# Performance work log

Measured on AMD Instinct MI355X. Metric: run time of the kernel, lower is better.

Reference implementation:

```python
import jax, jax.numpy as jnp
import numpy as np

E = 8          # num_experts
H = 2048       # hidden_size
D = 4096       # expert_dim
R = 8          # lora rank
SCALE = 16.0 / 8.0  # lora_alpha / r
T = 2048       # tokens per expert


def setup_inputs() -> dict:
    key = jax.random.key(0)
    ks = jax.random.split(key, 7)
    s = lambda *shape: 1.0 / np.sqrt(shape[-1])
    hidden_states = jax.random.normal(ks[0], (E * T, H), dtype=jnp.float32)
    # base weights (nn.Linear convention: [out, in]) stacked over experts
    W_gu = jax.random.normal(ks[1], (E, 2 * D, H), dtype=jnp.float32) * s(H)
    W_d = jax.random.normal(ks[2], (E, H, D), dtype=jnp.float32) * s(D)
    # LoRA factors: A [r, in] (kaiming-ish), B [out, r] (zeros in training init;
    # use small random here so the delta path is exercised)
    A_gu = jax.random.normal(ks[3], (E, R, H), dtype=jnp.float32) * s(H)
    B_gu = jax.random.normal(ks[4], (E, 2 * D, R), dtype=jnp.float32) * 0.01
    A_d = jax.random.normal(ks[5], (E, R, D), dtype=jnp.float32) * s(D)
    B_d = jax.random.normal(ks[6], (E, H, R), dtype=jnp.float32) * 0.01
    return {"hidden_states": hidden_states, "W_gu": W_gu, "A_gu": A_gu,
            "B_gu": B_gu, "W_d": W_d, "A_d": A_d, "B_d": B_d}


def _lora_linear(x, W, A, B):
    # x: [e, t, in]; W: [e, out, in]; A: [e, r, in]; B: [e, out, r]
    base = jnp.einsum('eti,eoi->eto', x, W)
    low = jnp.einsum('eti,eri->etr', x, A)        # skinny projection
    delta = jnp.einsum('etr,eor->eto', low, B)
    return base + SCALE * delta


def reference(hidden_states, W_gu, A_gu, B_gu, W_d, A_d, B_d):
    x = hidden_states.reshape(E, -1, H)           # [E, T, H]
    gate_up = _lora_linear(x, W_gu, A_gu, B_gu)   # [E, T, 2D]
    gate, up = gate_up[..., :D], gate_up[..., D:]
    h = up * jax.nn.silu(gate)                    # SwiGLU [E, T, D]
    out = _lora_linear(h, W_d, A_d, B_d)          # [E, T, H]
    return out.reshape(-1, H)
```

## Files before the change

### kernel.cpp

```cpp
#include <hip/hip_runtime.h>
#include <hip/hip_bf16.h>

#define E_ 8
#define H_ 2048
#define D_ 4096
#define R_ 8
#define T_ 2048
#define TWO_D_ 8192
#define SCALE_ 2.0f

typedef __attribute__((ext_vector_type(8))) short short8;
typedef __attribute__((ext_vector_type(4))) float f32x4;

__device__ __forceinline__ unsigned short f2bf(float f) {
  union { float f; unsigned u; } c; c.f = f;
  unsigned u = c.u + 0x7fffu + ((c.u >> 16) & 1u);
  return (unsigned short)(u >> 16);
}
__device__ __forceinline__ float bf2f(unsigned short s) {
  union { unsigned u; float f; } c; c.u = ((unsigned)s) << 16;
  return c.f;
}

__device__ __forceinline__ void gl16(const void* g, void* l) {
  __builtin_amdgcn_global_load_lds(
      (const __attribute__((address_space(1))) void*)g,
      (__attribute__((address_space(3))) void*)l, 16, 0, 0);
}

__device__ __forceinline__ int lds_off(int rr, int ks, int lq) {
  return (((rr >> 5) & 3) << 13) | (((rr >> 7) & 1) << 12) | ((rr & 31) << 7) | (ks << 6) | (lq << 4);
}

template <int K, bool XBF16, bool WRITEXB>
__global__ __launch_bounds__(256) void k_low(const void* __restrict__ Xv,
                                             const float* __restrict__ A,
                                             float* __restrict__ low,
                                             unsigned short* __restrict__ xbout) {
  int wave = (blockIdx.x * 256 + threadIdx.x) >> 6;
  int lane = threadIdx.x & 63;
  int e = wave >> 11;
  const float* Ae = A + (long)e * R_ * K;
  float acc[R_] = {0.f,0.f,0.f,0.f,0.f,0.f,0.f,0.f};
  for (int it = 0; it < K / 256; ++it) {
    int i = it * 256 + lane * 4;
    float xv[4];
    if constexpr (!XBF16) {
      const float* x = (const float*)Xv + (long)wave * K;
      f32x4 v = *(const f32x4*)(x + i);
      xv[0]=v[0]; xv[1]=v[1]; xv[2]=v[2]; xv[3]=v[3];
      if constexpr (WRITEXB) {
        ushort4 u; u.x=f2bf(xv[0]); u.y=f2bf(xv[1]); u.z=f2bf(xv[2]); u.w=f2bf(xv[3]);
        *(ushort4*)(xbout + (long)wave * K + i) = u;
      }
    } else {
      const unsigned short* x = (const unsigned short*)Xv + (long)wave * K;
      ushort4 u = *(const ushort4*)(x + i);
      xv[0]=bf2f(u.x); xv[1]=bf2f(u.y); xv[2]=bf2f(u.z); xv[3]=bf2f(u.w);
    }
    #pragma unroll
    for (int r = 0; r < R_; ++r) {
      f32x4 a = *(const f32x4*)(Ae + r * K + i);
      acc[r] += xv[0]*a[0] + xv[1]*a[1] + xv[2]*a[2] + xv[3]*a[3];
    }
  }
  #pragma unroll
  for (int r = 0; r < R_; ++r) {
    float v = acc[r];
    #pragma unroll
    for (int off = 32; off > 0; off >>= 1) v += __shfl_xor(v, off);
    acc[r] = v;
  }
  if (lane == 0) {
    #pragma unroll
    for (int r = 0; r < R_; ++r) low[(long)wave * R_ + r] = acc[r];
  }
}

__global__ __launch_bounds__(256) void k_f2bf(const float* __restrict__ src,
                                              unsigned short* __restrict__ dst,
                                              long n) {
  long i = ((long)blockIdx.x * 256 + threadIdx.x) * 8;
  long stride = (long)gridDim.x * 256 * 8;
  for (; i < n; i += stride) {
    f32x4 a = *(const f32x4*)(src + i);
    f32x4 b = *(const f32x4*)(src + i + 4);
    ushort4 lo, hi;
    lo.x=f2bf(a[0]); lo.y=f2bf(a[1]); lo.z=f2bf(a[2]); lo.w=f2bf(a[3]);
    hi.x=f2bf(b[0]); hi.y=f2bf(b[1]); hi.z=f2bf(b[2]); hi.w=f2bf(b[3]);
    *(ushort4*)(dst + i) = lo;
    *(ushort4*)(dst + i + 4) = hi;
  }
}

__global__ __launch_bounds__(512, 2) void k_gemm1_8p(
    const unsigned short* __restrict__ Xb, const unsigned short* __restrict__ Wb,
    const float* __restrict__ Bgu, const float* __restrict__ low,
    unsigned short* __restrict__ Hout) {
  __shared__ __align__(16) char lds[131072];

  const int MT = T_ / 256, NT = D_ / 128;
  int b = blockIdx.x;
  int cpx = (int)gridDim.x >> 3;
  int swz = (b & 7) * cpx + (b >> 3);
  int e  = swz / (MT * NT);
  int r0 = swz % (MT * NT);
  int nt = r0 / MT, mt = r0 % MT;

  int tid = threadIdx.x, lane = tid & 63;
  int wid = tid >> 6, wm = wid >> 2, wn = wid & 3;
  int lrow = lane & 15, lq = lane >> 4;
  int X4 = (lrow & 7) << 4;
  const int NKT = H_ / 64;

  unsigned ro = (unsigned)tid * 16;
  unsigned so = ro ^ (((ro >> 7) & 7u) << 4);
  int sh = (so >> 12) & 1, sr = (so >> 7) & 31, sc = (so & 127) >> 1;
  const unsigned short* pA[4]; const unsigned short* pB[4];
  #pragma unroll
  for (int q = 0; q < 4; ++q) {
    long arow = (long)e * T_ + mt * 256 + sh * 128 + q * 32 + sr;
    pA[q] = Xb + arow * H_ + sc;
    long wrow = sh ? ((long)e * TWO_D_ + D_ + nt * 128 + q * 32 + sr)
                   : ((long)e * TWO_D_ +      nt * 128 + q * 32 + sr);
    pB[q] = Wb + wrow * (long)H_ + sc;
  }
  auto SA = [&](int d, int q) { gl16(pA[q], lds + d * 32768 + q * 8192 + ro); pA[q] += 64; };
  auto SB = [&](int d, int q) { gl16(pB[q], lds + 65536 + d * 32768 + q * 8192 + ro); pB[q] += 64; };

  f32x4 accg[2][8] = {}, accu[2][8] = {};
  short8 BG[2][2], BU[2][2], af[2][2];

  SA(0,0); SB(0,0); SA(0,1); SB(0,1); SA(0,2); SB(0,2); SA(0,3); SB(0,3);
  SA(1,0); SB(1,0); SA(1,1); SB(1,1); SA(1,2); SB(1,2);
  asm volatile("s_waitcnt vmcnt(6)" ::: "memory");
  __builtin_amdgcn_s_barrier();

  int rbA = wm * 128 + lrow;
  for (int t = 0; t < NKT; ++t) {
    int d = t & 1;
    const char* Ab = lds + d * 32768;
    const char* Bb = lds + 65536 + d * 32768;

#define G1_MFMA(q)                                                                   \
    __builtin_amdgcn_s_setprio(1);                                                   \
    _Pragma("unroll") for (int m2 = 0; m2 < 2; ++m2)                                 \
      _Pragma("unroll") for (int ks = 0; ks < 2; ++ks)                               \
        _Pragma("unroll") for (int nj = 0; nj < 2; ++nj) {                           \
          accg[nj][(q)*2+m2] = __builtin_amdgcn_mfma_f32_16x16x32_bf16(              \
              BG[nj][ks], af[m2][ks], accg[nj][(q)*2+m2], 0, 0, 0);                  \
          accu[nj][(q)*2+m2] = __builtin_amdgcn_mfma_f32_16x16x32_bf16(              \
              BU[nj][ks], af[m2][ks], accu[nj][(q)*2+m2], 0, 0, 0);                  \
        }                                                                            \
    __builtin_amdgcn_s_setprio(0);

#define G1_LDA(q)                                                                    \
    _Pragma("unroll") for (int m2 = 0; m2 < 2; ++m2)                                 \
      _Pragma("unroll") for (int ks = 0; ks < 2; ++ks)                               \
        af[m2][ks] = *(const short8*)(Ab + (lds_off(rbA + ((q)*2+m2)*16, ks, lq) ^ X4));

#define G1_SYNC()                                                                    \
    __builtin_amdgcn_s_barrier();                                                    \
    asm volatile("s_waitcnt lgkmcnt(0)" ::: "memory");                               \
    __builtin_amdgcn_sched_barrier(0);

    #pragma unroll
    for (int nj = 0; nj < 2; ++nj)
      #pragma unroll
      for (int ks = 0; ks < 2; ++ks) {
        int rg = wn * 32 + nj * 16 + lrow;
        BG[nj][ks] = *(const short8*)(Bb + (lds_off(rg, ks, lq) ^ X4));
        BU[nj][ks] = *(const short8*)(Bb + (lds_off(rg + 128, ks, lq) ^ X4));
      }
    G1_LDA(0);
    if (t + 1 < NKT) { SA(d ^ 1, 3); SB(d ^ 1, 3); }
    G1_SYNC();
    G1_MFMA(0);
    __builtin_amdgcn_s_barrier();
    G1_LDA(1);
    if (t + 2 < NKT) { SA(d, 0); SB(d, 0); }
    G1_SYNC();
    G1_MFMA(1);
    __builtin_amdgcn_s_barrier();
    G1_LDA(2);
    if (t + 2 < NKT) { SA(d, 1); SB(d, 1); }
    G1_SYNC();
    G1_MFMA(2);
    __builtin_amdgcn_s_barrier();
    G1_LDA(3);
    if (t + 2 < NKT) {
      SA(d, 2); SB(d, 2);
      asm volatile("s_waitcnt vmcnt(6)" ::: "memory");
    } else {
      asm volatile("s_waitcnt vmcnt(0)" ::: "memory");
    }
    G1_SYNC();
    G1_MFMA(3);
    __builtin_amdgcn_s_barrier();
  }

  __syncthreads();
  unsigned short* sLo2 = (unsigned short*)lds;
  unsigned short* sB2  = (unsigned short*)(lds + 16384);
  {
    short8 z = {};
    if (tid < 256) {
      const float* lp = low + ((long)e * T_ + mt * 256 + tid) * R_;
      short8 v;
      #pragma unroll
      for (int r = 0; r < 8; ++r) ((unsigned short*)&v)[r] = f2bf(SCALE_ * lp[r]);
      *(short8*)(sLo2 + tid * 32) = v;
      *(short8*)(sLo2 + tid * 32 + 8) = z;
      *(short8*)(sLo2 + tid * 32 + 16) = z;
      *(short8*)(sLo2 + tid * 32 + 24) = z;
    } else {
      int r = tid - 256;
      long wrow = (r < 128) ? ((long)e * TWO_D_ + nt * 128 + r)
                            : ((long)e * TWO_D_ + D_ + nt * 128 + (r - 128));
      const float* bp = Bgu + wrow * R_;
      short8 v;
      #pragma unroll
      for (int k = 0; k < 8; ++k) ((unsigned short*)&v)[k] = f2bf(bp[k]);
      *(short8*)(sB2 + r * 32) = v;
      *(short8*)(sB2 + r * 32 + 8) = z;
      *(short8*)(sB2 + r * 32 + 16) = z;
      *(short8*)(sB2 + r * 32 + 24) = z;
    }
  }
  __syncthreads();
  {
    #pragma unroll
    for (int mi = 0; mi < 8; ++mi) {
      short8 alo = *(const short8*)(sLo2 + (rbA + mi * 16) * 32 + lq * 8);
      #pragma unroll
      for (int nj = 0; nj < 2; ++nj) {
        int rg = wn * 32 + nj * 16 + lrow;
        short8 bg2 = *(const short8*)(sB2 + rg * 32 + lq * 8);
        short8 bu2 = *(const short8*)(sB2 + (rg + 128) * 32 + lq * 8);
        accg[nj][mi] = __builtin_amdgcn_mfma_f32_16x16x32_bf16(bg2, alo, accg[nj][mi], 0, 0, 0);
        accu[nj][mi] = __builtin_amdgcn_mfma_f32_16x16x32_bf16(bu2, alo, accu[nj][mi], 0, 0, 0);
      }
    }
  }
  unsigned short* sT = (unsigned short*)(lds + 32768);
  #pragma unroll
  for (int mi = 0; mi < 8; ++mi) {
    int tl = rbA + mi * 16;
    #pragma unroll
    for (int nj = 0; nj < 2; ++nj) {
      int cb = wn * 32 + nj * 16 + lq * 4;
      ushort4 o;
      #pragma unroll
      for (int j = 0; j < 4; ++j) {
        float gate = accg[nj][mi][j];
        float up   = accu[nj][mi][j];
        float hh = up * (gate / (1.f + __expf(-gate)));
        (&o.x)[j] = f2bf(hh);
      }
      *(ushort4*)(sT + tl * 136 + cb) = o;
    }
  }
  __syncthreads();
  {
    long base = ((long)e * T_ + mt * 256) * D_ + nt * 128;
    int rr2 = tid >> 4, cc2 = (tid & 15) * 8;
    #pragma unroll
    for (int p = 0; p < 8; ++p) {
      int r = p * 32 + rr2;
      short8 v = *(const short8*)(sT + r * 136 + cc2);
      *(short8*)(Hout + base + (long)r * D_ + cc2) = v;
    }
  }
}

__global__ __launch_bounds__(512, 2) void k_gemm2_8p(
    const unsigned short* __restrict__ Hin, const unsigned short* __restrict__ Wdb,
    const float* __restrict__ Bd, const float* __restrict__ low,
    float* __restrict__ Out) {
  __shared__ __align__(16) char lds[131072];

  const int MT = T_ / 256, NT = H_ / 256;
  int b = blockIdx.x;
  int cpx = (int)gridDim.x >> 3;
  int swz = (b & 7) * cpx + (b >> 3);
  int e  = swz / (MT * NT);
  int r0 = swz % (MT * NT);
  int nt = r0 / MT, mt = r0 % MT;

  int tid = threadIdx.x, lane = tid & 63;
  int wid = tid >> 6, wm = wid >> 2, wn = wid & 3;
  int lrow = lane & 15, lq = lane >> 4;
  int X4 = (lrow & 7) << 4;
  const int NKT = D_ / 64;

  unsigned ro = (unsigned)tid * 16;
  unsigned so = ro ^ (((ro >> 7) & 7u) << 4);
  int sh = (so >> 12) & 1, sr = (so >> 7) & 31, sc = (so & 127) >> 1;
  const unsigned short* pA[4]; const unsigned short* pB[4];
  #pragma unroll
  for (int q = 0; q < 4; ++q) {
    long arow = (long)e * T_ + mt * 256 + sh * 128 + q * 32 + sr;
    pA[q] = Hin + arow * D_ + sc;
    long wrow = (long)e * H_ + nt * 256 + sh * 128 + q * 32 + sr;
    pB[q] = Wdb + wrow * (long)D_ + sc;
  }
  auto SA = [&](int d, int q) { gl16(pA[q], lds + d * 32768 + q * 8192 + ro); pA[q] += 64; };
  auto SB = [&](int d, int q) { gl16(pB[q], lds + 65536 + d * 32768 + q * 8192 + ro); pB[q] += 64; };

  f32x4 acc[8][4] = {};
  short8 BF[4][2], af[2][2];

  SA(0,0); SB(0,0); SA(0,1); SB(0,1); SA(0,2); SB(0,2); SA(0,3); SB(0,3);
  SA(1,0); SB(1,0); SA(1,1); SB(1,1); SA(1,2); SB(1,2);
  asm volatile("s_waitcnt vmcnt(6)" ::: "memory");
  __builtin_amdgcn_s_barrier();

  int rbA = wm * 128 + lrow;
  for (int t = 0; t < NKT; ++t) {
    int d = t & 1;
    const char* Ab = lds + d * 32768;
    const char* Bb = lds + 65536 + d * 32768;

#define G2_MFMA(q)                                                                   \
    __builtin_amdgcn_s_setprio(1);                                                   \
    _Pragma("unroll") for (int m2 = 0; m2 < 2; ++m2)                                 \
      _Pragma("unroll") for (int ks = 0; ks < 2; ++ks)                               \
        _Pragma("unroll") for (int ni = 0; ni < 4; ++ni)                             \
          acc[(q)*2+m2][ni] = __builtin_amdgcn_mfma_f32_16x16x32_bf16(               \
              af[m2][ks], BF[ni][ks], acc[(q)*2+m2][ni], 0, 0, 0);                   \
    __builtin_amdgcn_s_setprio(0);

#define G2_LDA(q)                                                                    \
    _Pragma("unroll") for (int m2 = 0; m2 < 2; ++m2)                                 \
      _Pragma("unroll") for (int ks = 0; ks < 2; ++ks)                               \
        af[m2][ks] = *(const short8*)(Ab + (lds_off(rbA + ((q)*2+m2)*16, ks, lq) ^ X4));

    #pragma unroll
    for (int ni = 0; ni < 4; ++ni)
      #pragma unroll
      for (int ks = 0; ks < 2; ++ks)
        BF[ni][ks] = *(const short8*)(Bb + (lds_off(wn * 64 + ni * 16 + lrow, ks, lq) ^ X4));
    G2_LDA(0);
    if (t + 1 < NKT) { SA(d ^ 1, 3); SB(d ^ 1, 3); }
    __builtin_amdgcn_s_barrier();
    asm volatile("s_waitcnt lgkmcnt(0)" ::: "memory");
    __builtin_amdgcn_sched_barrier(0);
    G2_MFMA(0);
    __builtin_amdgcn_s_barrier();
    G2_LDA(1);
    if (t + 2 < NKT) { SA(d, 0); SB(d, 0); }
    __builtin_amdgcn_s_barrier();
    asm volatile("s_waitcnt lgkmcnt(0)" ::: "memory");
    __builtin_amdgcn_sched_barrier(0);
    G2_MFMA(1);
    __builtin_amdgcn_s_barrier();
    G2_LDA(2);
    if (t + 2 < NKT) { SA(d, 1); SB(d, 1); }
    __builtin_amdgcn_s_barrier();
    asm volatile("s_waitcnt lgkmcnt(0)" ::: "memory");
    __builtin_amdgcn_sched_barrier(0);
    G2_MFMA(2);
    __builtin_amdgcn_s_barrier();
    G2_LDA(3);
    if (t + 2 < NKT) {
      SA(d, 2); SB(d, 2);
      asm volatile("s_waitcnt vmcnt(6)" ::: "memory");
    } else {
      asm volatile("s_waitcnt vmcnt(0)" ::: "memory");
    }
    __builtin_amdgcn_s_barrier();
    asm volatile("s_waitcnt lgkmcnt(0)" ::: "memory");
    __builtin_amdgcn_sched_barrier(0);
    G2_MFMA(3);
    __builtin_amdgcn_s_barrier();
  }

  __syncthreads();
  unsigned short* sLo2 = (unsigned short*)lds;
  unsigned short* sB2  = (unsigned short*)(lds + 16384);
  {
    short8 z = {};
    if (tid < 256) {
      const float* lp = low + ((long)e * T_ + mt * 256 + tid) * R_;
      short8 v;
      #pragma unroll
      for (int r = 0; r < 8; ++r) ((unsigned short*)&v)[r] = f2bf(SCALE_ * lp[r]);
      *(short8*)(sLo2 + tid * 32) = v;
      *(short8*)(sLo2 + tid * 32 + 8) = z;
      *(short8*)(sLo2 + tid * 32 + 16) = z;
      *(short8*)(sLo2 + tid * 32 + 24) = z;
    } else {
      int r = tid - 256;
      const float* bp = Bd + ((long)e * H_ + nt * 256 + r) * R_;
      short8 v;
      #pragma unroll
      for (int k = 0; k < 8; ++k) ((unsigned short*)&v)[k] = f2bf(bp[k]);
      *(short8*)(sB2 + r * 32) = v;
      *(short8*)(sB2 + r * 32 + 8) = z;
      *(short8*)(sB2 + r * 32 + 16) = z;
      *(short8*)(sB2 + r * 32 + 24) = z;
    }
  }
  __syncthreads();
  #pragma unroll
  for (int mi = 0; mi < 8; ++mi) {
    short8 alo = *(const short8*)(sLo2 + (rbA + mi * 16) * 32 + lq * 8);
    #pragma unroll
    for (int ni = 0; ni < 4; ++ni) {
      short8 bd2 = *(const short8*)(sB2 + (wn * 64 + ni * 16 + lrow) * 32 + lq * 8);
      acc[mi][ni] = __builtin_amdgcn_mfma_f32_16x16x32_bf16(alo, bd2, acc[mi][ni], 0, 0, 0);
    }
  }
  {
    long rowbase = (long)e * T_ + mt * 256 + wm * 128;
    int colbase = nt * 256 + wn * 64;
    #pragma unroll
    for (int mi = 0; mi < 8; ++mi)
      #pragma unroll
      for (int j = 0; j < 4; ++j) {
        long row = rowbase + mi * 16 + lq * 4 + j;
        #pragma unroll
        for (int ni = 0; ni < 4; ++ni)
          Out[row * H_ + colbase + ni * 16 + lrow] = acc[mi][ni][j];
      }
  }
}

extern "C" void kernel_launch(void* const* d_in, const int* in_sizes, int n_in,
                              void* d_out, int out_size, void* d_ws, size_t ws_size,
                              hipStream_t stream) {
  const float* x   = (const float*)d_in[0];
  const float* Wgu = (const float*)d_in[1];
  const float* Agu = (const float*)d_in[2];
  const float* Bgu = (const float*)d_in[3];
  const float* Wd  = (const float*)d_in[4];
  const float* Ad  = (const float*)d_in[5];
  const float* Bd  = (const float*)d_in[6];
  float* out = (float*)d_out;

  char* ws = (char*)d_ws;
  const size_t SZ_H   = (size_t)E_ * T_ * D_ * 2;
  const size_t SZ_LOW = (size_t)E_ * T_ * R_ * 4;
  const size_t SZ_XB  = (size_t)E_ * T_ * H_ * 2;
  const size_t SZ_WGU = (size_t)E_ * TWO_D_ * H_ * 2;

  unsigned short* hbuf = (unsigned short*)ws;
  float* low1 = (float*)(ws + SZ_H);
  float* low2 = (float*)(ws + SZ_H + SZ_LOW);
  unsigned short* xb   = (unsigned short*)(ws + SZ_H + 2 * SZ_LOW);
  unsigned short* wgub = (unsigned short*)(ws + SZ_H + 2 * SZ_LOW + SZ_XB);
  unsigned short* wdb  = (unsigned short*)(ws + SZ_H + 2 * SZ_LOW + SZ_XB + SZ_WGU);

  hipLaunchKernelGGL((k_low<H_, false, true>), dim3(E_ * T_ / 4), dim3(256), 0, stream,
                     (const void*)x, Agu, low1, xb);
  hipLaunchKernelGGL(k_f2bf, dim3(2048), dim3(256), 0, stream, Wgu, wgub, (long)E_ * TWO_D_ * H_);
  hipLaunchKernelGGL(k_f2bf, dim3(2048), dim3(256), 0, stream, Wd,  wdb,  (long)E_ * H_ * D_);
  hipLaunchKernelGGL(k_gemm1_8p, dim3(E_ * (T_ / 256) * (D_ / 128)), dim3(512), 0, stream,
                     xb, wgub, Bgu, low1, hbuf);
  hipLaunchKernelGGL((k_low<D_, true, false>), dim3(E_ * T_ / 4), dim3(256), 0, stream,
                     (const void*)hbuf, Ad, low2, (unsigned short*)nullptr);
  hipLaunchKernelGGL(k_gemm2_8p, dim3(E_ * (T_ / 256) * (H_ / 256)), dim3(512), 0, stream,
                     hbuf, wdb, Bd, low2, out);
}
```

Before: 1.129 ms.

## Fuse fp32-to-bf16 weight conversion into GEMM B-tile loads via registers

Drops the two standalone weight conversion kernels. Each GEMM now loads fp32 weight tiles into registers, converts them with packed bf16 convert instructions, and writes them to LDS inside a restructured software pipeline with adjusted vmcnt waits. This removes a full fp32 read plus bf16 write-and-reread of both weight tensors. In exchange, each GEMM block reads twice as many weight bytes, and weights are re-read and re-converted by every M-tile block (8 per expert), and register pressure rises.

```diff
diff --git a/kernel.cpp b/kernel.cpp
--- a/kernel.cpp
+++ b/kernel.cpp
@@ -77,24 +77,16 @@
   }
 }
 
-__global__ __launch_bounds__(256) void k_f2bf(const float* __restrict__ src,
-                                              unsigned short* __restrict__ dst,
-                                              long n) {
-  long i = ((long)blockIdx.x * 256 + threadIdx.x) * 8;
-  long stride = (long)gridDim.x * 256 * 8;
-  for (; i < n; i += stride) {
-    f32x4 a = *(const f32x4*)(src + i);
-    f32x4 b = *(const f32x4*)(src + i + 4);
-    ushort4 lo, hi;
-    lo.x=f2bf(a[0]); lo.y=f2bf(a[1]); lo.z=f2bf(a[2]); lo.w=f2bf(a[3]);
-    hi.x=f2bf(b[0]); hi.y=f2bf(b[1]); hi.z=f2bf(b[2]); hi.w=f2bf(b[3]);
-    *(ushort4*)(dst + i) = lo;
-    *(ushort4*)(dst + i + 4) = hi;
-  }
-}
+#define CVT_WR(S0, S1, DST)                                                         \
+  { uint4 wv;                                                                       \
+    asm("v_cvt_pk_bf16_f32 %0, %1, %2" : "=v"(wv.x) : "v"((S0)[0]), "v"((S0)[1]));  \
+    asm("v_cvt_pk_bf16_f32 %0, %1, %2" : "=v"(wv.y) : "v"((S0)[2]), "v"((S0)[3]));  \
+    asm("v_cvt_pk_bf16_f32 %0, %1, %2" : "=v"(wv.z) : "v"((S1)[0]), "v"((S1)[1]));  \
+    asm("v_cvt_pk_bf16_f32 %0, %1, %2" : "=v"(wv.w) : "v"((S1)[2]), "v"((S1)[3]));  \
+    *(uint4*)(DST) = wv; }
 
 __global__ __launch_bounds__(512, 2) void k_gemm1_8p(
-    const unsigned short* __restrict__ Xb, const unsigned short* __restrict__ Wb,
+    const unsigned short* __restrict__ Xb, const float* __restrict__ Wgu,
     const float* __restrict__ Bgu, const float* __restrict__ low,
     unsigned short* __restrict__ Hout) {
   __shared__ __align__(16) char lds[131072];
@@ -116,24 +108,43 @@
   unsigned ro = (unsigned)tid * 16;
   unsigned so = ro ^ (((ro >> 7) & 7u) << 4);
   int sh = (so >> 12) & 1, sr = (so >> 7) & 31, sc = (so & 127) >> 1;
-  const unsigned short* pA[4]; const unsigned short* pB[4];
+  const unsigned short* pA[4]; const float* pB[4];
   #pragma unroll
   for (int q = 0; q < 4; ++q) {
     long arow = (long)e * T_ + mt * 256 + sh * 128 + q * 32 + sr;
     pA[q] = Xb + arow * H_ + sc;
     long wrow = sh ? ((long)e * TWO_D_ + D_ + nt * 128 + q * 32 + sr)
                    : ((long)e * TWO_D_ +      nt * 128 + q * 32 + sr);
-    pB[q] = Wb + wrow * (long)H_ + sc;
+    pB[q] = Wgu + wrow * (long)H_ + sc;
   }
   auto SA = [&](int d, int q) { gl16(pA[q], lds + d * 32768 + q * 8192 + ro); pA[q] += 64; };
-  auto SB = [&](int d, int q) { gl16(pB[q], lds + 65536 + d * 32768 + q * 8192 + ro); pB[q] += 64; };
+
+  f32x4 bl[4][2];
+#define G1_IB(s, q) { bl[s][0] = *(const f32x4*)(pB[q]); bl[s][1] = *(const f32x4*)(pB[q] + 4); pB[q] += 64; }
+#define G1_WRB(s, dd, qq) CVT_WR(bl[s][0], bl[s][1], lds + 65536 + (dd) * 32768 + (qq) * 8192 + ro)
 
   f32x4 accg[2][8] = {}, accu[2][8] = {};
   short8 BG[2][2], BU[2][2], af[2][2];
 
-  SA(0,0); SB(0,0); SA(0,1); SB(0,1); SA(0,2); SB(0,2); SA(0,3); SB(0,3);
-  SA(1,0); SB(1,0); SA(1,1); SB(1,1); SA(1,2); SB(1,2);
-  asm volatile("s_waitcnt vmcnt(6)" ::: "memory");
+  {
+    f32x4 pr[7][2];
+    #pragma unroll
+    for (int q = 0; q < 4; ++q) {
+      pr[q][0] = *(const f32x4*)(pB[q]); pr[q][1] = *(const f32x4*)(pB[q] + 4); pB[q] += 64;
+      SA(0, q);
+    }
+    #pragma unroll
+    for (int q = 0; q < 3; ++q) {
+      pr[4 + q][0] = *(const f32x4*)(pB[q]); pr[4 + q][1] = *(const f32x4*)(pB[q] + 4); pB[q] += 64;
+      SA(1, q);
+    }
+    #pragma unroll
+    for (int i = 0; i < 7; ++i) {
+      int dd = (i < 4) ? 0 : 1, qq = (i < 4) ? i : i - 4;
+      CVT_WR(pr[i][0], pr[i][1], lds + 65536 + dd * 32768 + qq * 8192 + ro);
+    }
+  }
+  asm volatile("s_waitcnt vmcnt(0)" ::: "memory");
   __builtin_amdgcn_s_barrier();
 
   int rbA = wm * 128 + lrow;
@@ -164,6 +175,8 @@
     asm volatile("s_waitcnt lgkmcnt(0)" ::: "memory");                               \
     __builtin_amdgcn_sched_barrier(0);
 
+    if (t > 0 && t + 1 < NKT) { G1_WRB(1, d ^ 1, 0); }
+    if (t + 1 < NKT) { G1_IB(0, 3); SA(d ^ 1, 3); }
     #pragma unroll
     for (int nj = 0; nj < 2; ++nj)
       #pragma unroll
@@ -173,27 +186,29 @@
         BU[nj][ks] = *(const short8*)(Bb + (lds_off(rg + 128, ks, lq) ^ X4));
       }
     G1_LDA(0);
-    if (t + 1 < NKT) { SA(d ^ 1, 3); SB(d ^ 1, 3); }
     G1_SYNC();
     G1_MFMA(0);
     __builtin_amdgcn_s_barrier();
+    if (t > 0 && t + 1 < NKT) { G1_WRB(2, d ^ 1, 1); }
+    if (t + 2 < NKT) { G1_IB(1, 0); SA(d, 0); }
     G1_LDA(1);
-    if (t + 2 < NKT) { SA(d, 0); SB(d, 0); }
     G1_SYNC();
     G1_MFMA(1);
     __builtin_amdgcn_s_barrier();
+    if (t > 0 && t + 1 < NKT) { G1_WRB(3, d ^ 1, 2); }
+    if (t + 2 < NKT) { G1_IB(2, 1); SA(d, 1); }
     G1_LDA(2);
-    if (t + 2 < NKT) { SA(d, 1); SB(d, 1); }
     G1_SYNC();
     G1_MFMA(2);
     __builtin_amdgcn_s_barrier();
-    G1_LDA(3);
+    if (t + 1 < NKT) { G1_WRB(0, d ^ 1, 3); }
     if (t + 2 < NKT) {
-      SA(d, 2); SB(d, 2);
-      asm volatile("s_waitcnt vmcnt(6)" ::: "memory");
+      G1_IB(3, 2); SA(d, 2);
+      asm volatile("s_waitcnt vmcnt(9)" ::: "memory");
     } else {
       asm volatile("s_waitcnt vmcnt(0)" ::: "memory");
     }
+    G1_LDA(3);
     G1_SYNC();
     G1_MFMA(3);
     __builtin_amdgcn_s_barrier();
@@ -274,7 +289,7 @@
 }
 
 __global__ __launch_bounds__(512, 2) void k_gemm2_8p(
-    const unsigned short* __restrict__ Hin, const unsigned short* __restrict__ Wdb,
+    const unsigned short* __restrict__ Hin, const float* __restrict__ Wd,
     const float* __restrict__ Bd, const float* __restrict__ low,
     float* __restrict__ Out) {
   __shared__ __align__(16) char lds[131072];
@@ -296,23 +311,42 @@
   unsigned ro = (unsigned)tid * 16;
   unsigned so = ro ^ (((ro >> 7) & 7u) << 4);
   int sh = (so >> 12) & 1, sr = (so >> 7) & 31, sc = (so & 127) >> 1;
-  const unsigned short* pA[4]; const unsigned short* pB[4];
+  const unsigned short* pA[4]; const float* pB[4];
   #pragma unroll
   for (int q = 0; q < 4; ++q) {
     long arow = (long)e * T_ + mt * 256 + sh * 128 + q * 32 + sr;
     pA[q] = Hin + arow * D_ + sc;
     long wrow = (long)e * H_ + nt * 256 + sh * 128 + q * 32 + sr;
-    pB[q] = Wdb + wrow * (long)D_ + sc;
+    pB[q] = Wd + wrow * (long)D_ + sc;
   }
   auto SA = [&](int d, int q) { gl16(pA[q], lds + d * 32768 + q * 8192 + ro); pA[q] += 64; };
-  auto SB = [&](int d, int q) { gl16(pB[q], lds + 65536 + d * 32768 + q * 8192 + ro); pB[q] += 64; };
+
+  f32x4 bl[4][2];
+#define G2_IB(s, q) { bl[s][0] = *(const f32x4*)(pB[q]); bl[s][1] = *(const f32x4*)(pB[q] + 4); pB[q] += 64; }
+#define G2_WRB(s, dd, qq) CVT_WR(bl[s][0], bl[s][1], lds + 65536 + (dd) * 32768 + (qq) * 8192 + ro)
 
   f32x4 acc[8][4] = {};
   short8 BF[4][2], af[2][2];
 
-  SA(0,0); SB(0,0); SA(0,1); SB(0,1); SA(0,2); SB(0,2); SA(0,3); SB(0,3);
-  SA(1,0); SB(1,0); SA(1,1); SB(1,1); SA(1,2); SB(1,2);
-  asm volatile("s_waitcnt vmcnt(6)" ::: "memory");
+  {
+    f32x4 pr[7][2];
+    #pragma unroll
+    for (int q = 0; q < 4; ++q) {
+      pr[q][0] = *(const f32x4*)(pB[q]); pr[q][1] = *(const f32x4*)(pB[q] + 4); pB[q] += 64;
+      SA(0, q);
+    }
+    #pragma unroll
+    for (int q = 0; q < 3; ++q) {
+      pr[4 + q][0] = *(const f32x4*)(pB[q]); pr[4 + q][1] = *(const f32x4*)(pB[q] + 4); pB[q] += 64;
+      SA(1, q);
+    }
+    #pragma unroll
+    for (int i = 0; i < 7; ++i) {
+      int dd = (i < 4) ? 0 : 1, qq = (i < 4) ? i : i - 4;
+      CVT_WR(pr[i][0], pr[i][1], lds + 65536 + dd * 32768 + qq * 8192 + ro);
+    }
+  }
+  asm volatile("s_waitcnt vmcnt(0)" ::: "memory");
   __builtin_amdgcn_s_barrier();
 
   int rbA = wm * 128 + lrow;
@@ -335,42 +369,43 @@
       _Pragma("unroll") for (int ks = 0; ks < 2; ++ks)                               \
         af[m2][ks] = *(const short8*)(Ab + (lds_off(rbA + ((q)*2+m2)*16, ks, lq) ^ X4));
 
+#define G2_SYNC()                                                                    \
+    __builtin_amdgcn_s_barrier();                                                    \
+    asm volatile("s_waitcnt lgkmcnt(0)" ::: "memory");                               \
+    __builtin_amdgcn_sched_barrier(0);
+
+    if (t > 0 && t + 1 < NKT) { G2_WRB(1, d ^ 1, 0); }
+    if (t + 1 < NKT) { G2_IB(0, 3); SA(d ^ 1, 3); }
     #pragma unroll
     for (int ni = 0; ni < 4; ++ni)
       #pragma unroll
       for (int ks = 0; ks < 2; ++ks)
         BF[ni][ks] = *(const short8*)(Bb + (lds_off(wn * 64 + ni * 16 + lrow, ks, lq) ^ X4));
     G2_LDA(0);
-    if (t + 1 < NKT) { SA(d ^ 1, 3); SB(d ^ 1, 3); }
-    __builtin_amdgcn_s_barrier();
-    asm volatile("s_waitcnt lgkmcnt(0)" ::: "memory");
-    __builtin_amdgcn_sched_barrier(0);
+    G2_SYNC();
     G2_MFMA(0);
     __builtin_amdgcn_s_barrier();
+    if (t > 0 && t + 1 < NKT) { G2_WRB(2, d ^ 1, 1); }
+    if (t + 2 < NKT) { G2_IB(1, 0); SA(d, 0); }
     G2_LDA(1);
-    if (t + 2 < NKT) { SA(d, 0); SB(d, 0); }
-    __builtin_amdgcn_s_barrier();
-    asm volatile("s_waitcnt lgkmcnt(0)" ::: "memory");
-    __builtin_amdgcn_sched_barrier(0);
+    G2_SYNC();
     G2_MFMA(1);
     __builtin_amdgcn_s_barrier();
+    if (t > 0 && t + 1 < NKT) { G2_WRB(3, d ^ 1, 2); }
+    if (t + 2 < NKT) { G2_IB(2, 1); SA(d, 1); }
     G2_LDA(2);
-    if (t + 2 < NKT) { SA(d, 1); SB(d, 1); }
-    __builtin_amdgcn_s_barrier();
-    asm volatile("s_waitcnt lgkmcnt(0)" ::: "memory");
-    __builtin_amdgcn_sched_barrier(0);
+    G2_SYNC();
     G2_MFMA(2);
     __builtin_amdgcn_s_barrier();
-    G2_LDA(3);
+    if (t + 1 < NKT) { G2_WRB(0, d ^ 1, 3); }
     if (t + 2 < NKT) {
-      SA(d, 2); SB(d, 2);
-      asm volatile("s_waitcnt vmcnt(6)" ::: "memory");
+      G2_IB(3, 2); SA(d, 2);
+      asm volatile("s_waitcnt vmcnt(9)" ::: "memory");
     } else {
       asm volatile("s_waitcnt vmcnt(0)" ::: "memory");
     }
-    __builtin_amdgcn_s_barrier();
-    asm volatile("s_waitcnt lgkmcnt(0)" ::: "memory");
-    __builtin_amdgcn_sched_barrier(0);
+    G2_LDA(3);
+    G2_SYNC();
     G2_MFMA(3);
     __builtin_amdgcn_s_barrier();
   }
@@ -441,24 +476,18 @@
   char* ws = (char*)d_ws;
   const size_t SZ_H   = (size_t)E_ * T_ * D_ * 2;
   const size_t SZ_LOW = (size_t)E_ * T_ * R_ * 4;
-  const size_t SZ_XB  = (size_t)E_ * T_ * H_ * 2;
-  const size_t SZ_WGU = (size_t)E_ * TWO_D_ * H_ * 2;
 
   unsigned short* hbuf = (unsigned short*)ws;
   float* low1 = (float*)(ws + SZ_H);
   float* low2 = (float*)(ws + SZ_H + SZ_LOW);
   unsigned short* xb   = (unsigned short*)(ws + SZ_H + 2 * SZ_LOW);
-  unsigned short* wgub = (unsigned short*)(ws + SZ_H + 2 * SZ_LOW + SZ_XB);
-  unsigned short* wdb  = (unsigned short*)(ws + SZ_H + 2 * SZ_LOW + SZ_XB + SZ_WGU);
 
   hipLaunchKernelGGL((k_low<H_, false, true>), dim3(E_ * T_ / 4), dim3(256), 0, stream,
                      (const void*)x, Agu, low1, xb);
-  hipLaunchKernelGGL(k_f2bf, dim3(2048), dim3(256), 0, stream, Wgu, wgub, (long)E_ * TWO_D_ * H_);
-  hipLaunchKernelGGL(k_f2bf, dim3(2048), dim3(256), 0, stream, Wd,  wdb,  (long)E_ * H_ * D_);
   hipLaunchKernelGGL(k_gemm1_8p, dim3(E_ * (T_ / 256) * (D_ / 128)), dim3(512), 0, stream,
-                     xb, wgub, Bgu, low1, hbuf);
+                     xb, Wgu, Bgu, low1, hbuf);
   hipLaunchKernelGGL((k_low<D_, true, false>), dim3(E_ * T_ / 4), dim3(256), 0, stream,
                      (const void*)hbuf, Ad, low2, (unsigned short*)nullptr);
   hipLaunchKernelGGL(k_gemm2_8p, dim3(E_ * (T_ / 256) * (H_ / 256)), dim3(512), 0, stream,
-                     hbuf, wdb, Bd, low2, out);
-}
+                     hbuf, Wd, Bd, low2, out);
+}
```

After: 1.280 ms. +13.3%, slower.

## Overlap W_d bf16 conversion with gemm1 and merge preprocessing launches

Applied to the files above, without the earlier changes.

The standalone f32-to-bf16 conversion of W_d is removed. Each gemm1 thread now converts a slice of W_d inside its K-loop, loading one f32x4 and storing it as bf16 over sixteen iterations. The goal is to hide that memory-bound work under the MFMA-bound GEMM. The gate/up LoRA projection, the x conversion and the W_gu conversion are also fused into one launch that splits its blocks by role. The cost is extra VGPRs and memory traffic inside gemm1, which could reduce occupancy or disturb its load pipeline.

```diff
diff --git a/kernel.cpp b/kernel.cpp
--- a/kernel.cpp
+++ b/kernel.cpp
@@ -32,35 +32,73 @@
   return (((rr >> 5) & 3) << 13) | (((rr >> 7) & 1) << 12) | ((rr & 31) << 7) | (ks << 6) | (lq << 4);
 }
 
-template <int K, bool XBF16, bool WRITEXB>
-__global__ __launch_bounds__(256) void k_low(const void* __restrict__ Xv,
-                                             const float* __restrict__ A,
+__global__ __launch_bounds__(256) void k_pre(const float* __restrict__ x,
+                                             const float* __restrict__ Agu,
                                              float* __restrict__ low,
-                                             unsigned short* __restrict__ xbout) {
+                                             unsigned short* __restrict__ xb,
+                                             const float* __restrict__ Wgu,
+                                             unsigned short* __restrict__ wgub) {
+  const int NB_LOW = E_ * T_ / 4;
+  if (blockIdx.x < NB_LOW) {
+    int wave = (blockIdx.x * 256 + threadIdx.x) >> 6;
+    int lane = threadIdx.x & 63;
+    int e = wave >> 11;
+    const float* Ae = Agu + (long)e * R_ * H_;
+    float acc[R_] = {0.f,0.f,0.f,0.f,0.f,0.f,0.f,0.f};
+    for (int it = 0; it < H_ / 256; ++it) {
+      int i = it * 256 + lane * 4;
+      const float* xp = x + (long)wave * H_;
+      f32x4 v = *(const f32x4*)(xp + i);
+      ushort4 u; u.x=f2bf(v[0]); u.y=f2bf(v[1]); u.z=f2bf(v[2]); u.w=f2bf(v[3]);
+      *(ushort4*)(xb + (long)wave * H_ + i) = u;
+      #pragma unroll
+      for (int r = 0; r < R_; ++r) {
+        f32x4 a = *(const f32x4*)(Ae + r * H_ + i);
+        acc[r] += v[0]*a[0] + v[1]*a[1] + v[2]*a[2] + v[3]*a[3];
+      }
+    }
+    #pragma unroll
+    for (int r = 0; r < R_; ++r) {
+      float v = acc[r];
+      #pragma unroll
+      for (int off = 32; off > 0; off >>= 1) v += __shfl_xor(v, off);
+      acc[r] = v;
+    }
+    if (lane == 0) {
+      #pragma unroll
+      for (int r = 0; r < R_; ++r) low[(long)wave * R_ + r] = acc[r];
+    }
+  } else {
+    const long n = (long)E_ * TWO_D_ * H_;
+    long i = ((long)(blockIdx.x - NB_LOW) * 256 + threadIdx.x) * 8;
+    const long stride = (long)1024 * 256 * 8;
+    for (; i < n; i += stride) {
+      f32x4 a = *(const f32x4*)(Wgu + i);
+      f32x4 b = *(const f32x4*)(Wgu + i + 4);
+      ushort4 lo, hi;
+      lo.x=f2bf(a[0]); lo.y=f2bf(a[1]); lo.z=f2bf(a[2]); lo.w=f2bf(a[3]);
+      hi.x=f2bf(b[0]); hi.y=f2bf(b[1]); hi.z=f2bf(b[2]); hi.w=f2bf(b[3]);
+      *(ushort4*)(wgub + i) = lo;
+      *(ushort4*)(wgub + i + 4) = hi;
+    }
+  }
+}
+
+__global__ __launch_bounds__(256) void k_low2(const unsigned short* __restrict__ Hb,
+                                              const float* __restrict__ Ad,
+                                              float* __restrict__ low) {
   int wave = (blockIdx.x * 256 + threadIdx.x) >> 6;
   int lane = threadIdx.x & 63;
   int e = wave >> 11;
-  const float* Ae = A + (long)e * R_ * K;
+  const float* Ae = Ad + (long)e * R_ * D_;
   float acc[R_] = {0.f,0.f,0.f,0.f,0.f,0.f,0.f,0.f};
-  for (int it = 0; it < K / 256; ++it) {
+  for (int it = 0; it < D_ / 256; ++it) {
     int i = it * 256 + lane * 4;
-    float xv[4];
-    if constexpr (!XBF16) {
-      const float* x = (const float*)Xv + (long)wave * K;
-      f32x4 v = *(const f32x4*)(x + i);
-      xv[0]=v[0]; xv[1]=v[1]; xv[2]=v[2]; xv[3]=v[3];
-      if constexpr (WRITEXB) {
-        ushort4 u; u.x=f2bf(xv[0]); u.y=f2bf(xv[1]); u.z=f2bf(xv[2]); u.w=f2bf(xv[3]);
-        *(ushort4*)(xbout + (long)wave * K + i) = u;
-      }
-    } else {
-      const unsigned short* x = (const unsigned short*)Xv + (long)wave * K;
-      ushort4 u = *(const ushort4*)(x + i);
-      xv[0]=bf2f(u.x); xv[1]=bf2f(u.y); xv[2]=bf2f(u.z); xv[3]=bf2f(u.w);
-    }
+    ushort4 u = *(const ushort4*)(Hb + (long)wave * D_ + i);
+    float xv[4] = {bf2f(u.x), bf2f(u.y), bf2f(u.z), bf2f(u.w)};
     #pragma unroll
     for (int r = 0; r < R_; ++r) {
-      f32x4 a = *(const f32x4*)(Ae + r * K + i);
+      f32x4 a = *(const f32x4*)(Ae + r * D_ + i);
       acc[r] += xv[0]*a[0] + xv[1]*a[1] + xv[2]*a[2] + xv[3]*a[3];
     }
   }
@@ -77,26 +115,11 @@
   }
 }
 
-__global__ __launch_bounds__(256) void k_f2bf(const float* __restrict__ src,
-                                              unsigned short* __restrict__ dst,
-                                              long n) {
-  long i = ((long)blockIdx.x * 256 + threadIdx.x) * 8;
-  long stride = (long)gridDim.x * 256 * 8;
-  for (; i < n; i += stride) {
-    f32x4 a = *(const f32x4*)(src + i);
-    f32x4 b = *(const f32x4*)(src + i + 4);
-    ushort4 lo, hi;
-    lo.x=f2bf(a[0]); lo.y=f2bf(a[1]); lo.z=f2bf(a[2]); lo.w=f2bf(a[3]);
-    hi.x=f2bf(b[0]); hi.y=f2bf(b[1]); hi.z=f2bf(b[2]); hi.w=f2bf(b[3]);
-    *(ushort4*)(dst + i) = lo;
-    *(ushort4*)(dst + i + 4) = hi;
-  }
-}
-
 __global__ __launch_bounds__(512, 2) void k_gemm1_8p(
     const unsigned short* __restrict__ Xb, const unsigned short* __restrict__ Wb,
     const float* __restrict__ Bgu, const float* __restrict__ low,
-    unsigned short* __restrict__ Hout) {
+    unsigned short* __restrict__ Hout,
+    const float* __restrict__ WdSrc, unsigned short* __restrict__ WdDst) {
   __shared__ __align__(16) char lds[131072];
 
   const int MT = T_ / 256, NT = D_ / 128;
@@ -112,6 +135,7 @@
   int lrow = lane & 15, lq = lane >> 4;
   int X4 = (lrow & 7) << 4;
   const int NKT = H_ / 64;
+  const long cid = (long)blockIdx.x * 512 + tid;
 
   unsigned ro = (unsigned)tid * 16;
   unsigned so = ro ^ (((ro >> 7) & 7u) << 4);
@@ -130,6 +154,7 @@
 
   f32x4 accg[2][8] = {}, accu[2][8] = {};
   short8 BG[2][2], BU[2][2], af[2][2];
+  f32x4 cr;
 
   SA(0,0); SB(0,0); SA(0,1); SB(0,1); SA(0,2); SB(0,2); SA(0,3); SB(0,3);
   SA(1,0); SB(1,0); SA(1,1); SB(1,1); SA(1,2); SB(1,2);
@@ -194,6 +219,13 @@
     } else {
       asm volatile("s_waitcnt vmcnt(0)" ::: "memory");
     }
+    if (t >= 2 && t <= 17) {
+      ushort4 o; o.x = f2bf(cr[0]); o.y = f2bf(cr[1]); o.z = f2bf(cr[2]); o.w = f2bf(cr[3]);
+      *(ushort4*)(WdDst + ((long)(t - 2) * 1048576 + cid) * 4) = o;
+    }
+    if (t >= 1 && t <= 16) {
+      cr = *(const f32x4*)(WdSrc + ((long)(t - 1) * 1048576 + cid) * 4);
+    }
     G1_SYNC();
     G1_MFMA(3);
     __builtin_amdgcn_s_barrier();
@@ -451,14 +483,11 @@
   unsigned short* wgub = (unsigned short*)(ws + SZ_H + 2 * SZ_LOW + SZ_XB);
   unsigned short* wdb  = (unsigned short*)(ws + SZ_H + 2 * SZ_LOW + SZ_XB + SZ_WGU);
 
-  hipLaunchKernelGGL((k_low<H_, false, true>), dim3(E_ * T_ / 4), dim3(256), 0, stream,
-                     (const void*)x, Agu, low1, xb);
-  hipLaunchKernelGGL(k_f2bf, dim3(2048), dim3(256), 0, stream, Wgu, wgub, (long)E_ * TWO_D_ * H_);
-  hipLaunchKernelGGL(k_f2bf, dim3(2048), dim3(256), 0, stream, Wd,  wdb,  (long)E_ * H_ * D_);
+  hipLaunchKernelGGL(k_pre, dim3(E_ * T_ / 4 + 1024), dim3(256), 0, stream,
+                     x, Agu, low1, xb, Wgu, wgub);
   hipLaunchKernelGGL(k_gemm1_8p, dim3(E_ * (T_ / 256) * (D_ / 128)), dim3(512), 0, stream,
-                     xb, wgub, Bgu, low1, hbuf);
-  hipLaunchKernelGGL((k_low<D_, true, false>), dim3(E_ * T_ / 4), dim3(256), 0, stream,
-                     (const void*)hbuf, Ad, low2, (unsigned short*)nullptr);
+                     xb, wgub, Bgu, low1, hbuf, Wd, wdb);
+  hipLaunchKernelGGL(k_low2, dim3(E_ * T_ / 4), dim3(256), 0, stream, hbuf, Ad, low2);
   hipLaunchKernelGGL(k_gemm2_8p, dim3(E_ * (T_ / 256) * (H_ / 256)), dim3(512), 0, stream,
                      hbuf, wdb, Bd, low2, out);
 }
```

Result: slower. 1.171 ms (+3.7%).

## Fold LoRA factors into bf16 weights during conversion, drop low-rank passes

Applied to the files above, without the earlier changes.

Computes W + scale·B·A while converting the expert weights to bf16 in one fused preprocessing kernel, also absorbing the activation conversion. This removes both skinny low-rank projection kernels (including the full reread of the intermediate activation) and the rank-8 MFMA epilogues in both GEMMs, and cuts launch count. The LoRA delta is now rounded into the bf16 weight, slightly changing numerics.

```diff
diff --git a/kernel.cpp b/kernel.cpp
--- a/kernel.cpp
+++ b/kernel.cpp
@@ -17,10 +17,6 @@
   unsigned u = c.u + 0x7fffu + ((c.u >> 16) & 1u);
   return (unsigned short)(u >> 16);
 }
-__device__ __forceinline__ float bf2f(unsigned short s) {
-  union { unsigned u; float f; } c; c.u = ((unsigned)s) << 16;
-  return c.f;
-}
 
 __device__ __forceinline__ void gl16(const void* g, void* l) {
   __builtin_amdgcn_global_load_lds(
@@ -32,70 +28,101 @@
   return (((rr >> 5) & 3) << 13) | (((rr >> 7) & 1) << 12) | ((rr & 31) << 7) | (ks << 6) | (lq << 4);
 }
 
-template <int K, bool XBF16, bool WRITEXB>
-__global__ __launch_bounds__(256) void k_low(const void* __restrict__ Xv,
-                                             const float* __restrict__ A,
-                                             float* __restrict__ low,
-                                             unsigned short* __restrict__ xbout) {
-  int wave = (blockIdx.x * 256 + threadIdx.x) >> 6;
-  int lane = threadIdx.x & 63;
-  int e = wave >> 11;
-  const float* Ae = A + (long)e * R_ * K;
-  float acc[R_] = {0.f,0.f,0.f,0.f,0.f,0.f,0.f,0.f};
-  for (int it = 0; it < K / 256; ++it) {
-    int i = it * 256 + lane * 4;
-    float xv[4];
-    if constexpr (!XBF16) {
-      const float* x = (const float*)Xv + (long)wave * K;
-      f32x4 v = *(const f32x4*)(x + i);
-      xv[0]=v[0]; xv[1]=v[1]; xv[2]=v[2]; xv[3]=v[3];
-      if constexpr (WRITEXB) {
-        ushort4 u; u.x=f2bf(xv[0]); u.y=f2bf(xv[1]); u.z=f2bf(xv[2]); u.w=f2bf(xv[3]);
-        *(ushort4*)(xbout + (long)wave * K + i) = u;
+__global__ __launch_bounds__(256) void k_pre(const float* __restrict__ x,
+                                             unsigned short* __restrict__ xb,
+                                             const float* __restrict__ Wgu,
+                                             const float* __restrict__ Agu,
+                                             const float* __restrict__ Bgu,
+                                             unsigned short* __restrict__ wgub,
+                                             const float* __restrict__ Wd,
+                                             const float* __restrict__ Ad,
+                                             const float* __restrict__ Bd,
+                                             unsigned short* __restrict__ wdb) {
+  const int NB_X = 1024, NB_GU = 8192;
+  int bb = blockIdx.x, tid = threadIdx.x;
+  if (bb < NB_X) {
+    const long n = (long)E_ * T_ * H_;
+    long i = ((long)bb * 256 + tid) * 8;
+    const long stride = (long)NB_X * 256 * 8;
+    for (; i < n; i += stride) {
+      f32x4 a = *(const f32x4*)(x + i);
+      f32x4 b = *(const f32x4*)(x + i + 4);
+      ushort4 lo, hi;
+      lo.x=f2bf(a[0]); lo.y=f2bf(a[1]); lo.z=f2bf(a[2]); lo.w=f2bf(a[3]);
+      hi.x=f2bf(b[0]); hi.y=f2bf(b[1]); hi.z=f2bf(b[2]); hi.w=f2bf(b[3]);
+      *(ushort4*)(xb + i) = lo;
+      *(ushort4*)(xb + i + 4) = hi;
+    }
+  } else if (bb < NB_X + NB_GU) {
+    int b2 = bb - NB_X;
+    int e = b2 >> 10;
+    int o8 = (b2 & 1023) * 8;
+    int c = tid * 8;
+    f32x4 a0[8], a1[8];
+    #pragma unroll
+    for (int r = 0; r < 8; ++r) {
+      const float* ap = Agu + ((long)e * R_ + r) * H_ + c;
+      a0[r] = *(const f32x4*)ap;
+      a1[r] = *(const f32x4*)(ap + 4);
+    }
+    #pragma unroll
+    for (int o = 0; o < 8; ++o) {
+      long row = (long)e * TWO_D_ + o8 + o;
+      const float* bp = Bgu + row * R_;
+      const float* wp = Wgu + row * (long)H_ + c;
+      f32x4 w0 = *(const f32x4*)wp;
+      f32x4 w1 = *(const f32x4*)(wp + 4);
+      #pragma unroll
+      for (int r = 0; r < 8; ++r) {
+        float s = SCALE_ * bp[r];
+        w0 += s * a0[r];
+        w1 += s * a1[r];
       }
-    } else {
-      const unsigned short* x = (const unsigned short*)Xv + (long)wave * K;
-      ushort4 u = *(const ushort4*)(x + i);
-      xv[0]=bf2f(u.x); xv[1]=bf2f(u.y); xv[2]=bf2f(u.z); xv[3]=bf2f(u.w);
-    }
-    #pragma unroll
-    for (int r = 0; r < R_; ++r) {
-      f32x4 a = *(const f32x4*)(Ae + r * K + i);
-      acc[r] += xv[0]*a[0] + xv[1]*a[1] + xv[2]*a[2] + xv[3]*a[3];
-    }
-  }
-  #pragma unroll
-  for (int r = 0; r < R_; ++r) {
-    float v = acc[r];
-    #pragma unroll
-    for (int off = 32; off > 0; off >>= 1) v += __shfl_xor(v, off);
-    acc[r] = v;
-  }
-  if (lane == 0) {
-    #pragma unroll
-    for (int r = 0; r < R_; ++r) low[(long)wave * R_ + r] = acc[r];
-  }
-}
-
-__global__ __launch_bounds__(256) void k_f2bf(const float* __restrict__ src,
-                                              unsigned short* __restrict__ dst,
-                                              long n) {
-  long i = ((long)blockIdx.x * 256 + threadIdx.x) * 8;
-  long stride = (long)gridDim.x * 256 * 8;
-  for (; i < n; i += stride) {
-    f32x4 a = *(const f32x4*)(src + i);
-    f32x4 b = *(const f32x4*)(src + i + 4);
-    ushort4 lo, hi;
-    lo.x=f2bf(a[0]); lo.y=f2bf(a[1]); lo.z=f2bf(a[2]); lo.w=f2bf(a[3]);
-    hi.x=f2bf(b[0]); hi.y=f2bf(b[1]); hi.z=f2bf(b[2]); hi.w=f2bf(b[3]);
-    *(ushort4*)(dst + i) = lo;
-    *(ushort4*)(dst + i + 4) = hi;
+      ushort4 lo, hi;
+      lo.x=f2bf(w0[0]); lo.y=f2bf(w0[1]); lo.z=f2bf(w0[2]); lo.w=f2bf(w0[3]);
+      hi.x=f2bf(w1[0]); hi.y=f2bf(w1[1]); hi.z=f2bf(w1[2]); hi.w=f2bf(w1[3]);
+      unsigned short* op = wgub + row * (long)H_ + c;
+      *(ushort4*)op = lo;
+      *(ushort4*)(op + 4) = hi;
+    }
+  } else {
+    int b2 = bb - NB_X - NB_GU;
+    int e = b2 >> 9;
+    int rem = b2 & 511;
+    int h8 = (rem >> 1) * 8;
+    int c = (rem & 1) * 2048 + tid * 8;
+    f32x4 a0[8], a1[8];
+    #pragma unroll
+    for (int r = 0; r < 8; ++r) {
+      const float* ap = Ad + ((long)e * R_ + r) * D_ + c;
+      a0[r] = *(const f32x4*)ap;
+      a1[r] = *(const f32x4*)(ap + 4);
+    }
+    #pragma unroll
+    for (int o = 0; o < 8; ++o) {
+      long row = (long)e * H_ + h8 + o;
+      const float* bp = Bd + row * R_;
+      const float* wp = Wd + row * (long)D_ + c;
+      f32x4 w0 = *(const f32x4*)wp;
+      f32x4 w1 = *(const f32x4*)(wp + 4);
+      #pragma unroll
+      for (int r = 0; r < 8; ++r) {
+        float s = SCALE_ * bp[r];
+        w0 += s * a0[r];
+        w1 += s * a1[r];
+      }
+      ushort4 lo, hi;
+      lo.x=f2bf(w0[0]); lo.y=f2bf(w0[1]); lo.z=f2bf(w0[2]); lo.w=f2bf(w0[3]);
+      hi.x=f2bf(w1[0]); hi.y=f2bf(w1[1]); hi.z=f2bf(w1[2]); hi.w=f2bf(w1[3]);
+      unsigned short* op = wdb + row * (long)D_ + c;
+      *(ushort4*)op = lo;
+      *(ushort4*)(op + 4) = hi;
+    }
   }
 }
 
 __global__ __launch_bounds__(512, 2) void k_gemm1_8p(
     const unsigned short* __restrict__ Xb, const unsigned short* __restrict__ Wb,
-    const float* __restrict__ Bgu, const float* __restrict__ low,
     unsigned short* __restrict__ Hout) {
   __shared__ __align__(16) char lds[131072];
 
@@ -200,48 +227,6 @@
   }
 
   __syncthreads();
-  unsigned short* sLo2 = (unsigned short*)lds;
-  unsigned short* sB2  = (unsigned short*)(lds + 16384);
-  {
-    short8 z = {};
-    if (tid < 256) {
-      const float* lp = low + ((long)e * T_ + mt * 256 + tid) * R_;
-      short8 v;
-      #pragma unroll
-      for (int r = 0; r < 8; ++r) ((unsigned short*)&v)[r] = f2bf(SCALE_ * lp[r]);
-      *(short8*)(sLo2 + tid * 32) = v;
-      *(short8*)(sLo2 + tid * 32 + 8) = z;
-      *(short8*)(sLo2 + tid * 32 + 16) = z;
-      *(short8*)(sLo2 + tid * 32 + 24) = z;
-    } else {
-      int r = tid - 256;
-      long wrow = (r < 128) ? ((long)e * TWO_D_ + nt * 128 + r)
-                            : ((long)e * TWO_D_ + D_ + nt * 128 + (r - 128));
-      const float* bp = Bgu + wrow * R_;
-      short8 v;
-      #pragma unroll
-      for (int k = 0; k < 8; ++k) ((unsigned short*)&v)[k] = f2bf(bp[k]);
-      *(short8*)(sB2 + r * 32) = v;
-      *(short8*)(sB2 + r * 32 + 8) = z;
-      *(short8*)(sB2 + r * 32 + 16) = z;
-      *(short8*)(sB2 + r * 32 + 24) = z;
-    }
-  }
-  __syncthreads();
-  {
-    #pragma unroll
-    for (int mi = 0; mi < 8; ++mi) {
-      short8 alo = *(const short8*)(sLo2 + (rbA + mi * 16) * 32 + lq * 8);
-      #pragma unroll
-      for (int nj = 0; nj < 2; ++nj) {
-        int rg = wn * 32 + nj * 16 + lrow;
-        short8 bg2 = *(const short8*)(sB2 + rg * 32 + lq * 8);
-        short8 bu2 = *(const short8*)(sB2 + (rg + 128) * 32 + lq * 8);
-        accg[nj][mi] = __builtin_amdgcn_mfma_f32_16x16x32_bf16(bg2, alo, accg[nj][mi], 0, 0, 0);
-        accu[nj][mi] = __builtin_amdgcn_mfma_f32_16x16x32_bf16(bu2, alo, accu[nj][mi], 0, 0, 0);
-      }
-    }
-  }
   unsigned short* sT = (unsigned short*)(lds + 32768);
   #pragma unroll
   for (int mi = 0; mi < 8; ++mi) {
@@ -275,7 +260,6 @@
 
 __global__ __launch_bounds__(512, 2) void k_gemm2_8p(
     const unsigned short* __restrict__ Hin, const unsigned short* __restrict__ Wdb,
-    const float* __restrict__ Bd, const float* __restrict__ low,
     float* __restrict__ Out) {
   __shared__ __align__(16) char lds[131072];
 
@@ -375,42 +359,6 @@
     __builtin_amdgcn_s_barrier();
   }
 
-  __syncthreads();
-  unsigned short* sLo2 = (unsigned short*)lds;
-  unsigned short* sB2  = (unsigned short*)(lds + 16384);
-  {
-    short8 z = {};
-    if (tid < 256) {
-      const float* lp = low + ((long)e * T_ + mt * 256 + tid) * R_;
-      short8 v;
-      #pragma unroll
-      for (int r = 0; r < 8; ++r) ((unsigned short*)&v)[r] = f2bf(SCALE_ * lp[r]);
-      *(short8*)(sLo2 + tid * 32) = v;
-      *(short8*)(sLo2 + tid * 32 + 8) = z;
-      *(short8*)(sLo2 + tid * 32 + 16) = z;
-      *(short8*)(sLo2 + tid * 32 + 24) = z;
-    } else {
-      int r = tid - 256;
-      const float* bp = Bd + ((long)e * H_ + nt * 256 + r) * R_;
-      short8 v;
-      #pragma unroll
-      for (int k = 0; k < 8; ++k) ((unsigned short*)&v)[k] = f2bf(bp[k]);
-      *(short8*)(sB2 + r * 32) = v;
-      *(short8*)(sB2 + r * 32 + 8) = z;
-      *(short8*)(sB2 + r * 32 + 16) = z;
-      *(short8*)(sB2 + r * 32 + 24) = z;
-    }
-  }
-  __syncthreads();
-  #pragma unroll
-  for (int mi = 0; mi < 8; ++mi) {
-    short8 alo = *(const short8*)(sLo2 + (rbA + mi * 16) * 32 + lq * 8);
-    #pragma unroll
-    for (int ni = 0; ni < 4; ++ni) {
-      short8 bd2 = *(const short8*)(sB2 + (wn * 64 + ni * 16 + lrow) * 32 + lq * 8);
-      acc[mi][ni] = __builtin_amdgcn_mfma_f32_16x16x32_bf16(alo, bd2, acc[mi][ni], 0, 0, 0);
-    }
-  }
   {
     long rowbase = (long)e * T_ + mt * 256 + wm * 128;
     int colbase = nt * 256 + wn * 64;
@@ -445,20 +393,14 @@
   const size_t SZ_WGU = (size_t)E_ * TWO_D_ * H_ * 2;
 
   unsigned short* hbuf = (unsigned short*)ws;
-  float* low1 = (float*)(ws + SZ_H);
-  float* low2 = (float*)(ws + SZ_H + SZ_LOW);
   unsigned short* xb   = (unsigned short*)(ws + SZ_H + 2 * SZ_LOW);
   unsigned short* wgub = (unsigned short*)(ws + SZ_H + 2 * SZ_LOW + SZ_XB);
   unsigned short* wdb  = (unsigned short*)(ws + SZ_H + 2 * SZ_LOW + SZ_XB + SZ_WGU);
 
-  hipLaunchKernelGGL((k_low<H_, false, true>), dim3(E_ * T_ / 4), dim3(256), 0, stream,
-                     (const void*)x, Agu, low1, xb);
-  hipLaunchKernelGGL(k_f2bf, dim3(2048), dim3(256), 0, stream, Wgu, wgub, (long)E_ * TWO_D_ * H_);
-  hipLaunchKernelGGL(k_f2bf, dim3(2048), dim3(256), 0, stream, Wd,  wdb,  (long)E_ * H_ * D_);
+  hipLaunchKernelGGL(k_pre, dim3(1024 + 8192 + 4096), dim3(256), 0, stream,
+                     x, xb, Wgu, Agu, Bgu, wgub, Wd, Ad, Bd, wdb);
   hipLaunchKernelGGL(k_gemm1_8p, dim3(E_ * (T_ / 256) * (D_ / 128)), dim3(512), 0, stream,
-                     xb, wgub, Bgu, low1, hbuf);
-  hipLaunchKernelGGL((k_low<D_, true, false>), dim3(E_ * T_ / 4), dim3(256), 0, stream,
-                     (const void*)hbuf, Ad, low2, (unsigned short*)nullptr);
+                     xb, wgub, hbuf);
   hipLaunchKernelGGL(k_gemm2_8p, dim3(E_ * (T_ / 256) * (H_ / 256)), dim3(512), 0, stream,
-                     hbuf, wdb, Bd, low2, out);
-}
+                     hbuf, wdb, out);
+}
```

Measured after the change: 1.002 ms. 1.13x faster.
